# Performance work log

Measured on AMD Instinct MI355X. Metric: run time of the kernel, lower is better.

Reference implementation:

```python
import jax, jax.numpy as jnp
import numpy as np

ALPHA = 0.2        # LeakyReLU slope
NEG_BIG = -9e15    # mask fill value from the original module


def setup_inputs() -> dict:
    key = jax.random.key(0)
    k1, k2, k3, k4 = jax.random.split(key, 4)
    N, F_IN, F_OUT = 8192, 256, 128
    h = jax.random.normal(k1, (N, F_IN), dtype=jnp.float32)
    adj = jax.random.randint(k2, (N, N), 0, 2, dtype=jnp.int32)
    W = jax.random.normal(k3, (F_IN, F_OUT), dtype=jnp.float32) * (1.0 / np.sqrt(F_IN))
    a = jax.random.normal(k4, (2 * F_OUT, 1), dtype=jnp.float32) * (1.0 / np.sqrt(2 * F_OUT))
    return {"h": h, "adj": adj, "W": W, "a": a}


def reference(h, adj, W, a):
    f_out = W.shape[1]
    Wh = h @ W                                   # [N, F_out]
    Wh1 = Wh @ a[:f_out, :]                      # [N, 1]
    Wh2 = Wh @ a[f_out:, :]                      # [N, 1]
    e = Wh1 + Wh2.T                              # [N, N] broadcast-add
    e = jnp.where(e > 0, e, ALPHA * e)           # LeakyReLU
    e = jnp.where(adj > 0, e, NEG_BIG)           # adjacency mask
    attention = jax.nn.softmax(e, axis=-1)       # row softmax
    # dropout rate = 0.0 -> identity
    h_prime = attention @ Wh                     # [N, F_out]
    return jax.nn.elu(h_prime)
```

## Files before the change

kernel.cpp:

```cpp
#include <hip/hip_runtime.h>

#define NV 8192
#define FIN 256
#define FOUT 128
#define NSPLIT 8
#define SPLITW 1024
#define NW32 256

typedef __bf16 bf16_t;
typedef __attribute__((ext_vector_type(8))) __bf16 bf16x8;
typedef __attribute__((ext_vector_type(16))) float f32x16;

__global__ __launch_bounds__(256) void pack_kernel(
    const int* __restrict__ adj, unsigned* __restrict__ bits)
{
  const int g0 = (blockIdx.x * 256 + threadIdx.x) * 4;
  unsigned ob[4];
  #pragma unroll
  for (int k = 0; k < 4; k++) {
    const int* src = adj + (size_t)(g0 + k) * 32;
    unsigned b = 0;
    #pragma unroll
    for (int q = 0; q < 8; q++) {
      int4 v = *(const int4*)(src + q * 4);
      b |= (v.x > 0) ? (1u << (q * 4 + 0)) : 0u;
      b |= (v.y > 0) ? (1u << (q * 4 + 1)) : 0u;
      b |= (v.z > 0) ? (1u << (q * 4 + 2)) : 0u;
      b |= (v.w > 0) ? (1u << (q * 4 + 3)) : 0u;
    }
    ob[k] = b;
  }
  uint4 o = make_uint4(ob[0], ob[1], ob[2], ob[3]);
  *(uint4*)(bits + g0) = o;
}

__global__ __launch_bounds__(256) void wh_kernel(
    const float* __restrict__ h, const float* __restrict__ W,
    const float* __restrict__ a,
    bf16_t* __restrict__ WhbT,
    float* __restrict__ E1, float* __restrict__ F1,
    float* __restrict__ E2, float* __restrict__ F2)
{
  __shared__ float As[64][34];
  __shared__ float Bs[64][128];
  __shared__ float Cs[32][129];
  __shared__ float red1[32][16];
  __shared__ float red2[32][16];
  const int t  = threadIdx.x;
  const int i0 = blockIdx.x * 32;
  const int c  = t & 15;
  const int r  = t >> 4;
  float acc0[8], acc1[8];
  #pragma unroll
  for (int j = 0; j < 8; j++) { acc0[j] = 0.f; acc1[j] = 0.f; }

  for (int k0 = 0; k0 < FIN; k0 += 64) {
    {
      const int ia = t >> 3;
      const int ka = (t & 7) * 8;
      const float* src = h + (size_t)(i0 + ia) * FIN + k0 + ka;
      float4 v0 = *(const float4*)src;
      float4 v1 = *(const float4*)(src + 4);
      As[ka+0][ia]=v0.x; As[ka+1][ia]=v0.y; As[ka+2][ia]=v0.z; As[ka+3][ia]=v0.w;
      As[ka+4][ia]=v1.x; As[ka+5][ia]=v1.y; As[ka+6][ia]=v1.z; As[ka+7][ia]=v1.w;
    }
    {
      const int kb = t >> 2;
      const int cb = (t & 3) * 32;
      const float4* src = (const float4*)(W + (size_t)(k0 + kb) * FOUT + cb);
      float4* dst = (float4*)&Bs[kb][cb];
      #pragma unroll
      for (int q = 0; q < 8; q++) dst[q] = src[q];
    }
    __syncthreads();
    #pragma unroll 4
    for (int k = 0; k < 64; k++) {
      float2 av = *(const float2*)&As[k][r*2];
      float b[8];
      *(float4*)&b[0] = *(const float4*)&Bs[k][c*8];
      *(float4*)&b[4] = *(const float4*)&Bs[k][c*8+4];
      #pragma unroll
      for (int j = 0; j < 8; j++) {
        acc0[j] = fmaf(av.x, b[j], acc0[j]);
        acc1[j] = fmaf(av.y, b[j], acc1[j]);
      }
    }
    __syncthreads();
  }

  float p1a = 0.f, p2a = 0.f, p1b = 0.f, p2b = 0.f;
  #pragma unroll
  for (int j = 0; j < 8; j++) {
    Cs[r*2][c*8+j]   = acc0[j];
    Cs[r*2+1][c*8+j] = acc1[j];
    float w1 = a[c*8+j];
    float w2 = a[FOUT + c*8+j];
    p1a = fmaf(acc0[j], w1, p1a); p2a = fmaf(acc0[j], w2, p2a);
    p1b = fmaf(acc1[j], w1, p1b); p2b = fmaf(acc1[j], w2, p2b);
  }
  red1[r*2][c]   = p1a; red2[r*2][c]   = p2a;
  red1[r*2+1][c] = p1b; red2[r*2+1][c] = p2b;
  __syncthreads();
  if (t < 32) {
    float s = 0.f;
    #pragma unroll
    for (int q = 0; q < 16; q++) s += red1[t][q];
    E1[i0 + t] = __expf(s);
    F1[i0 + t] = __expf(0.2f * s);
  } else if (t < 64) {
    float s = 0.f;
    #pragma unroll
    for (int q = 0; q < 16; q++) s += red2[t-32][q];
    E2[i0 + t - 32] = __expf(s);
    F2[i0 + t - 32] = __expf(0.2f * s);
  }
  {
    const int f = t & 127, half = t >> 7;
    union { bf16_t b[16]; uint4 v[2]; } pk;
    #pragma unroll
    for (int q = 0; q < 16; q++) pk.b[q] = (bf16_t)Cs[half*16 + q][f];
    uint4* dst = (uint4*)(WhbT + (size_t)f * NV + i0 + half*16);
    dst[0] = pk.v[0]; dst[1] = pk.v[1];
  }
}

__global__ __launch_bounds__(256, 3) void attn_kernel(
    const unsigned* __restrict__ abits, const bf16_t* __restrict__ WhbT,
    const float* __restrict__ E1v, const float* __restrict__ F1v,
    const float* __restrict__ E2v, const float* __restrict__ F2v,
    float* __restrict__ nump, float* __restrict__ denp)
{
  __shared__ bf16_t Plds[64][72];
  __shared__ bf16_t Blds[2][128][72];
  __shared__ float denlds[64][4];
  const int t     = threadIdx.x;
  const int rb    = blockIdx.x >> 3;
  const int split = blockIdx.x & 7;
  const int i0 = rb * 64;
  const int j0 = split * SPLITW;
  const int il = t >> 2;
  const int jg = (t & 3) * 16;
  const float e1 = E1v[i0 + il];
  const float f1 = F1v[i0 + il];
  const int lane = t & 63;
  const int w    = t >> 6;
  const int rh = (w & 1) * 32;
  const int ch = (w >> 1) * 64;
  const int ml = lane & 31;
  const int kh = (lane >> 5) * 8;
  const int bb = jg & 16;
  f32x16 acc0 = {};
  f32x16 acc1 = {};
  float den_t = 0.f;

  const int bn  = t >> 1;
  const int bhf = (t & 1) * 32;
  const bf16_t* bsrc = WhbT + (size_t)bn * NV + j0 + bhf;
  const unsigned* arow32 = abits + (size_t)(i0 + il) * NW32 + ((j0 + jg) >> 5);

  uint4 br0, br1, br2, br3;
  {
    const uint4* s4 = (const uint4*)bsrc;
    br0 = s4[0]; br1 = s4[1]; br2 = s4[2]; br3 = s4[3];
  }
  unsigned cbits = arow32[0];

  for (int jc = 0; jc < SPLITW; jc += 64) {
    const int jb  = j0 + jc;
    const int buf = (jc >> 6) & 1;
    {
      uint4* bd = (uint4*)&Blds[buf][bn][bhf];
      bd[0] = br0; bd[1] = br1; bd[2] = br2; bd[3] = br3;
    }
    float4 w0 = *(const float4*)(E2v + jb + jg);
    float4 w1 = *(const float4*)(E2v + jb + jg + 4);
    float4 w2 = *(const float4*)(E2v + jb + jg + 8);
    float4 w3 = *(const float4*)(E2v + jb + jg + 12);
    float4 x0 = *(const float4*)(F2v + jb + jg);
    float4 x1 = *(const float4*)(F2v + jb + jg + 4);
    float4 x2 = *(const float4*)(F2v + jb + jg + 8);
    float4 x3 = *(const float4*)(F2v + jb + jg + 12);
    const int jn = (jc + 64 < SPLITW) ? jc + 64 : jc;
    {
      const uint4* s4 = (const uint4*)(bsrc + jn);
      br0 = s4[0]; br1 = s4[1]; br2 = s4[2]; br3 = s4[3];
    }
    unsigned nbits = arow32[jn >> 5];
    {
      const unsigned hb = cbits >> bb;
      bf16x8 pv0, pv1;
      float d0 = 0.f, d1 = 0.f, d2 = 0.f, d3 = 0.f;
      #define PGRP(B, E4, F4, DD, PV, SL) { \
        float px = fmaxf(e1*E4.x, f1*F4.x); px = (hb & (1u<<(B+0))) ? px : 0.f; DD += px; PV[SL+0] = (bf16_t)px; \
        float py = fmaxf(e1*E4.y, f1*F4.y); py = (hb & (1u<<(B+1))) ? py : 0.f; DD += py; PV[SL+1] = (bf16_t)py; \
        float pz = fmaxf(e1*E4.z, f1*F4.z); pz = (hb & (1u<<(B+2))) ? pz : 0.f; DD += pz; PV[SL+2] = (bf16_t)pz; \
        float pw = fmaxf(e1*E4.w, f1*F4.w); pw = (hb & (1u<<(B+3))) ? pw : 0.f; DD += pw; PV[SL+3] = (bf16_t)pw; }
      PGRP( 0, w0, x0, d0, pv0, 0)
      PGRP( 4, w1, x1, d1, pv0, 4)
      PGRP( 8, w2, x2, d2, pv1, 0)
      PGRP(12, w3, x3, d3, pv1, 4)
      #undef PGRP
      den_t += (d0 + d1) + (d2 + d3);
      *(bf16x8*)&Plds[il][jg]     = pv0;
      *(bf16x8*)&Plds[il][jg + 8] = pv1;
    }
    asm volatile("s_waitcnt lgkmcnt(0)\n\ts_barrier" ::: "memory");
    #pragma unroll
    for (int ks = 0; ks < 4; ks++) {
      const int k = ks * 16 + kh;
      bf16x8 af = *(const bf16x8*)&Plds[rh + ml][k];
      bf16x8 b0 = *(const bf16x8*)&Blds[buf][ch + ml][k];
      bf16x8 b1 = *(const bf16x8*)&Blds[buf][ch + 32 + ml][k];
      acc0 = __builtin_amdgcn_mfma_f32_32x32x16_bf16(af, b0, acc0, 0, 0, 0);
      acc1 = __builtin_amdgcn_mfma_f32_32x32x16_bf16(af, b1, acc1, 0, 0, 0);
    }
    asm volatile("s_barrier" ::: "memory");
    cbits = nbits;
  }

  denlds[il][t & 3] = den_t;
  __syncthreads();
  if (t < 64) {
    denp[(size_t)split * NV + i0 + t] =
        denlds[t][0] + denlds[t][1] + denlds[t][2] + denlds[t][3];
  }
  float* base = nump + ((size_t)split * NV + i0) * FOUT;
  const int col = ch + ml;
  const int r4  = 4 * (lane >> 5);
  #pragma unroll
  for (int reg = 0; reg < 16; reg++) {
    const int row = rh + (reg & 3) + 8 * (reg >> 2) + r4;
    base[(size_t)row * FOUT + col]      = acc0[reg];
    base[(size_t)row * FOUT + col + 32] = acc1[reg];
  }
}

__global__ __launch_bounds__(256) void finalize_kernel(
    const float* __restrict__ nump, const float* __restrict__ denp,
    float* __restrict__ out)
{
  const int gid = blockIdx.x * 256 + threadIdx.x;
  const int i  = gid >> 5;
  const int f0 = (gid & 31) * 4;
  float den = 0.f;
  #pragma unroll
  for (int sp = 0; sp < NSPLIT; sp++) den += denp[(size_t)sp * NV + i];
  float4 s = make_float4(0.f, 0.f, 0.f, 0.f);
  #pragma unroll
  for (int sp = 0; sp < NSPLIT; sp++) {
    float4 v = *(const float4*)&nump[((size_t)sp * NV + i) * FOUT + f0];
    s.x += v.x; s.y += v.y; s.z += v.z; s.w += v.w;
  }
  const float inv = 1.0f / den;
  float4 r;
  r.x = s.x * inv; r.y = s.y * inv; r.z = s.z * inv; r.w = s.w * inv;
  r.x = r.x > 0.f ? r.x : __expf(r.x) - 1.0f;
  r.y = r.y > 0.f ? r.y : __expf(r.y) - 1.0f;
  r.z = r.z > 0.f ? r.z : __expf(r.z) - 1.0f;
  r.w = r.w > 0.f ? r.w : __expf(r.w) - 1.0f;
  *(float4*)&out[(size_t)i * FOUT + f0] = r;
}

extern "C" void kernel_launch(void* const* d_in, const int* in_sizes, int n_in,
                              void* d_out, int out_size, void* d_ws, size_t ws_size,
                              hipStream_t stream) {
  const float* h  = (const float*)d_in[0];
  const int*  adj = (const int*)d_in[1];
  const float* W  = (const float*)d_in[2];
  const float* a  = (const float*)d_in[3];
  float* out = (float*)d_out;
  char* ws = (char*)d_ws;
  bf16_t* WhbT = (bf16_t*)ws;
  float* E1   = (float*)(ws + 2097152);
  float* F1   = (float*)(ws + 2129920);
  float* E2   = (float*)(ws + 2162688);
  float* F2   = (float*)(ws + 2195456);
  float* denp = (float*)(ws + 2228224);
  float* nump = (float*)(ws + 2490368);
  unsigned* AdjBits = (unsigned*)(ws + 2490368 + 33554432);

  pack_kernel<<<2048, 256, 0, stream>>>(adj, AdjBits);
  wh_kernel<<<256, 256, 0, stream>>>(h, W, a, WhbT, E1, F1, E2, F2);
  attn_kernel<<<1024, 256, 0, stream>>>(AdjBits, WhbT, E1, F1, E2, F2, nump, denp);
  finalize_kernel<<<1024, 256, 0, stream>>>(nump, denp, out);
}
```

Before: 459.1 us.

## Compute attention P in MFMA A-fragment registers and read B directly from global

```diff
diff --git a/kernel.cpp b/kernel.cpp
--- a/kernel.cpp
+++ b/kernel.cpp
@@ -124,114 +124,79 @@
   }
 }
 
-__global__ __launch_bounds__(256, 3) void attn_kernel(
+__global__ __launch_bounds__(256, 2) void attn_kernel(
     const unsigned* __restrict__ abits, const bf16_t* __restrict__ WhbT,
     const float* __restrict__ E1v, const float* __restrict__ F1v,
     const float* __restrict__ E2v, const float* __restrict__ F2v,
     float* __restrict__ nump, float* __restrict__ denp)
 {
-  __shared__ bf16_t Plds[64][72];
-  __shared__ bf16_t Blds[2][128][72];
-  __shared__ float denlds[64][4];
   const int t     = threadIdx.x;
   const int rb    = blockIdx.x >> 3;
   const int split = blockIdx.x & 7;
-  const int i0 = rb * 64;
+  const int i0 = rb * 128;
   const int j0 = split * SPLITW;
-  const int il = t >> 2;
-  const int jg = (t & 3) * 16;
-  const float e1 = E1v[i0 + il];
-  const float f1 = F1v[i0 + il];
   const int lane = t & 63;
   const int w    = t >> 6;
-  const int rh = (w & 1) * 32;
-  const int ch = (w >> 1) * 64;
-  const int ml = lane & 31;
-  const int kh = (lane >> 5) * 8;
-  const int bb = jg & 16;
-  f32x16 acc0 = {};
-  f32x16 acc1 = {};
+  const int ml   = lane & 31;
+  const int kh   = (lane >> 5) * 8;
+  const int row  = i0 + w * 32 + ml;
+  const float e1 = E1v[row];
+  const float f1 = F1v[row];
+  f32x16 acc0 = {}, acc1 = {}, acc2 = {}, acc3 = {};
   float den_t = 0.f;
 
-  const int bn  = t >> 1;
-  const int bhf = (t & 1) * 32;
-  const bf16_t* bsrc = WhbT + (size_t)bn * NV + j0 + bhf;
-  const unsigned* arow32 = abits + (size_t)(i0 + il) * NW32 + ((j0 + jg) >> 5);
-
-  uint4 br0, br1, br2, br3;
-  {
-    const uint4* s4 = (const uint4*)bsrc;
-    br0 = s4[0]; br1 = s4[1]; br2 = s4[2]; br3 = s4[3];
-  }
-  unsigned cbits = arow32[0];
+  const unsigned* brow = abits + (size_t)row * NW32 + (j0 >> 5);
+  const bf16_t* bcol0 = WhbT + (size_t)(ml)      * NV + j0;
+  const bf16_t* bcol1 = WhbT + (size_t)(32 + ml) * NV + j0;
+  const bf16_t* bcol2 = WhbT + (size_t)(64 + ml) * NV + j0;
+  const bf16_t* bcol3 = WhbT + (size_t)(96 + ml) * NV + j0;
 
   for (int jc = 0; jc < SPLITW; jc += 64) {
-    const int jb  = j0 + jc;
-    const int buf = (jc >> 6) & 1;
-    {
-      uint4* bd = (uint4*)&Blds[buf][bn][bhf];
-      bd[0] = br0; bd[1] = br1; bd[2] = br2; bd[3] = br3;
-    }
-    float4 w0 = *(const float4*)(E2v + jb + jg);
-    float4 w1 = *(const float4*)(E2v + jb + jg + 4);
-    float4 w2 = *(const float4*)(E2v + jb + jg + 8);
-    float4 w3 = *(const float4*)(E2v + jb + jg + 12);
-    float4 x0 = *(const float4*)(F2v + jb + jg);
-    float4 x1 = *(const float4*)(F2v + jb + jg + 4);
-    float4 x2 = *(const float4*)(F2v + jb + jg + 8);
-    float4 x3 = *(const float4*)(F2v + jb + jg + 12);
-    const int jn = (jc + 64 < SPLITW) ? jc + 64 : jc;
-    {
-      const uint4* s4 = (const uint4*)(bsrc + jn);
-      br0 = s4[0]; br1 = s4[1]; br2 = s4[2]; br3 = s4[3];
-    }
-    unsigned nbits = arow32[jn >> 5];
-    {
-      const unsigned hb = cbits >> bb;
-      bf16x8 pv0, pv1;
-      float d0 = 0.f, d1 = 0.f, d2 = 0.f, d3 = 0.f;
-      #define PGRP(B, E4, F4, DD, PV, SL) { \
-        float px = fmaxf(e1*E4.x, f1*F4.x); px = (hb & (1u<<(B+0))) ? px : 0.f; DD += px; PV[SL+0] = (bf16_t)px; \
-        float py = fmaxf(e1*E4.y, f1*F4.y); py = (hb & (1u<<(B+1))) ? py : 0.f; DD += py; PV[SL+1] = (bf16_t)py; \
-        float pz = fmaxf(e1*E4.z, f1*F4.z); pz = (hb & (1u<<(B+2))) ? pz : 0.f; DD += pz; PV[SL+2] = (bf16_t)pz; \
-        float pw = fmaxf(e1*E4.w, f1*F4.w); pw = (hb & (1u<<(B+3))) ? pw : 0.f; DD += pw; PV[SL+3] = (bf16_t)pw; }
-      PGRP( 0, w0, x0, d0, pv0, 0)
-      PGRP( 4, w1, x1, d1, pv0, 4)
-      PGRP( 8, w2, x2, d2, pv1, 0)
-      PGRP(12, w3, x3, d3, pv1, 4)
-      #undef PGRP
-      den_t += (d0 + d1) + (d2 + d3);
-      *(bf16x8*)&Plds[il][jg]     = pv0;
-      *(bf16x8*)&Plds[il][jg + 8] = pv1;
-    }
-    asm volatile("s_waitcnt lgkmcnt(0)\n\ts_barrier" ::: "memory");
+    const uint2 bw = *(const uint2*)(brow + (jc >> 5));
     #pragma unroll
     for (int ks = 0; ks < 4; ks++) {
-      const int k = ks * 16 + kh;
-      bf16x8 af = *(const bf16x8*)&Plds[rh + ml][k];
-      bf16x8 b0 = *(const bf16x8*)&Blds[buf][ch + ml][k];
-      bf16x8 b1 = *(const bf16x8*)&Blds[buf][ch + 32 + ml][k];
-      acc0 = __builtin_amdgcn_mfma_f32_32x32x16_bf16(af, b0, acc0, 0, 0, 0);
-      acc1 = __builtin_amdgcn_mfma_f32_32x32x16_bf16(af, b1, acc1, 0, 0, 0);
-    }
-    asm volatile("s_barrier" ::: "memory");
-    cbits = nbits;
-  }
-
-  denlds[il][t & 3] = den_t;
-  __syncthreads();
-  if (t < 64) {
-    denp[(size_t)split * NV + i0 + t] =
-        denlds[t][0] + denlds[t][1] + denlds[t][2] + denlds[t][3];
+      const int jj = jc + ks * 16 + kh;
+      float4 e4a = *(const float4*)(E2v + j0 + jj);
+      float4 e4b = *(const float4*)(E2v + j0 + jj + 4);
+      float4 f4a = *(const float4*)(F2v + j0 + jj);
+      float4 f4b = *(const float4*)(F2v + j0 + jj + 4);
+      const int bi = ks * 16 + kh;
+      const unsigned wd = (bi & 32) ? bw.y : bw.x;
+      const unsigned hb = wd >> (bi & 31);
+      bf16x8 pa;
+      float p;
+      p = fmaxf(e1*e4a.x, f1*f4a.x); p = (hb &   1u) ? p : 0.f; den_t += p; pa[0] = (bf16_t)p;
+      p = fmaxf(e1*e4a.y, f1*f4a.y); p = (hb &   2u) ? p : 0.f; den_t += p; pa[1] = (bf16_t)p;
+      p = fmaxf(e1*e4a.z, f1*f4a.z); p = (hb &   4u) ? p : 0.f; den_t += p; pa[2] = (bf16_t)p;
+      p = fmaxf(e1*e4a.w, f1*f4a.w); p = (hb &   8u) ? p : 0.f; den_t += p; pa[3] = (bf16_t)p;
+      p = fmaxf(e1*e4b.x, f1*f4b.x); p = (hb &  16u) ? p : 0.f; den_t += p; pa[4] = (bf16_t)p;
+      p = fmaxf(e1*e4b.y, f1*f4b.y); p = (hb &  32u) ? p : 0.f; den_t += p; pa[5] = (bf16_t)p;
+      p = fmaxf(e1*e4b.z, f1*f4b.z); p = (hb &  64u) ? p : 0.f; den_t += p; pa[6] = (bf16_t)p;
+      p = fmaxf(e1*e4b.w, f1*f4b.w); p = (hb & 128u) ? p : 0.f; den_t += p; pa[7] = (bf16_t)p;
+      bf16x8 b0 = *(const bf16x8*)(bcol0 + jj);
+      bf16x8 b1 = *(const bf16x8*)(bcol1 + jj);
+      bf16x8 b2 = *(const bf16x8*)(bcol2 + jj);
+      bf16x8 b3 = *(const bf16x8*)(bcol3 + jj);
+      acc0 = __builtin_amdgcn_mfma_f32_32x32x16_bf16(pa, b0, acc0, 0, 0, 0);
+      acc1 = __builtin_amdgcn_mfma_f32_32x32x16_bf16(pa, b1, acc1, 0, 0, 0);
+      acc2 = __builtin_amdgcn_mfma_f32_32x32x16_bf16(pa, b2, acc2, 0, 0, 0);
+      acc3 = __builtin_amdgcn_mfma_f32_32x32x16_bf16(pa, b3, acc3, 0, 0, 0);
+    }
+  }
+
+  const float den_full = den_t + __shfl_xor(den_t, 32);
+  if (lane < 32) {
+    denp[(size_t)split * NV + row] = den_full;
   }
   float* base = nump + ((size_t)split * NV + i0) * FOUT;
-  const int col = ch + ml;
-  const int r4  = 4 * (lane >> 5);
+  const int r4 = 4 * (lane >> 5);
   #pragma unroll
   for (int reg = 0; reg < 16; reg++) {
-    const int row = rh + (reg & 3) + 8 * (reg >> 2) + r4;
-    base[(size_t)row * FOUT + col]      = acc0[reg];
-    base[(size_t)row * FOUT + col + 32] = acc1[reg];
+    const int crow = w * 32 + (reg & 3) + 8 * (reg >> 2) + r4;
+    base[(size_t)crow * FOUT + ml]      = acc0[reg];
+    base[(size_t)crow * FOUT + ml + 32] = acc1[reg];
+    base[(size_t)crow * FOUT + ml + 64] = acc2[reg];
+    base[(size_t)crow * FOUT + ml + 96] = acc3[reg];
   }
 }
 
@@ -281,6 +246,6 @@
 
   pack_kernel<<<2048, 256, 0, stream>>>(adj, AdjBits);
   wh_kernel<<<256, 256, 0, stream>>>(h, W, a, WhbT, E1, F1, E2, F2);
-  attn_kernel<<<1024, 256, 0, stream>>>(AdjBits, WhbT, E1, F1, E2, F2, nump, denp);
+  attn_kernel<<<512, 256, 0, stream>>>(AdjBits, WhbT, E1, F1, E2, F2, nump, denp);
   finalize_kernel<<<1024, 256, 0, stream>>>(nump, denp, out);
 }
```

New measurement: 488.2 us. 1.06x slower.
